# Kernel tuning notes

Measured on AMD Instinct MI355X. Metric: run time of the kernel, lower is better.

Reference implementation:

```python
import jax, jax.numpy as jnp
import numpy as np
from jax import lax

# Model dims (match init_kwargs / Mamba2 defaults)
B = 8; C_IN = 512; C_OUT = 512; H = 32; W = 32; L = H * W
D_STATE = 64; D_CONV = 4; EXPAND = 2; HEADDIM = 64
D_INNER = EXPAND * C_IN            # 1024
NHEADS = D_INNER // HEADDIM        # 16
D_XBC = D_INNER + 2 * D_STATE      # 1152 (ngroups=1)
D_IN_PROJ = 2 * D_INNER + 2 * D_STATE + NHEADS
EPS = 1e-5


def setup_inputs() -> dict:
    key = jax.random.key(0)
    ks = jax.random.split(key, 16)
    x = jax.random.normal(ks[0], (B, C_IN, H, W), jnp.float32)
    ln_w = jnp.ones((C_IN,), jnp.float32)
    ln_b = jnp.zeros((C_IN,), jnp.float32)
    in_proj_w = jax.random.normal(ks[1], (D_IN_PROJ, C_IN), jnp.float32) * 0.02
    conv1d_w = jax.random.normal(ks[2], (D_XBC, D_CONV), jnp.float32) * 0.2
    conv1d_b = jax.random.normal(ks[3], (D_XBC,), jnp.float32) * 0.02
    dt0 = jax.random.uniform(ks[4], (NHEADS,), jnp.float32, 1e-3, 0.1)
    dt_bias = jnp.log(jnp.expm1(dt0))  # inverse softplus init
    A_log = jnp.log(jax.random.uniform(ks[5], (NHEADS,), jnp.float32, 1.0, 16.0))
    D = jax.random.normal(ks[6], (NHEADS,), jnp.float32)
    rms_w = jnp.ones((D_INNER,), jnp.float32)
    out_proj_w = jax.random.normal(ks[7], (C_IN, D_INNER), jnp.float32) * 0.02
    conv2d_w = jax.random.normal(ks[8], (C_OUT, C_IN), jnp.float32) * 0.04
    conv2d_b = jnp.zeros((C_OUT,), jnp.float32)
    bn_g = jnp.ones((C_OUT,), jnp.float32)
    bn_b = jnp.zeros((C_OUT,), jnp.float32)
    bn_mean = jnp.zeros((C_OUT,), jnp.float32)
    bn_var = jnp.ones((C_OUT,), jnp.float32)
    return dict(x=x, ln_w=ln_w, ln_b=ln_b, in_proj_w=in_proj_w, conv1d_w=conv1d_w,
                conv1d_b=conv1d_b, dt_bias=dt_bias, A_log=A_log, D=D, rms_w=rms_w,
                out_proj_w=out_proj_w, conv2d_w=conv2d_w, conv2d_b=conv2d_b,
                bn_g=bn_g, bn_b=bn_b, bn_mean=bn_mean, bn_var=bn_var)


def reference(x, ln_w, ln_b, in_proj_w, conv1d_w, conv1d_b, dt_bias, A_log, D,
              rms_w, out_proj_w, conv2d_w, conv2d_b, bn_g, bn_b, bn_mean, bn_var):
    Bb, C, Hh, Ww = x.shape
    Ltok = Hh * Ww
    # tokens: (B, L, C)
    t = x.reshape(Bb, C, Ltok).transpose(0, 2, 1)
    # LayerNorm over channel dim
    mu = jnp.mean(t, -1, keepdims=True)
    var = jnp.mean(jnp.square(t - mu), -1, keepdims=True)
    xn = (t - mu) * lax.rsqrt(var + EPS) * ln_w + ln_b
    # Mamba2 in_proj -> [z, xBC, dt]
    zxbcdt = jnp.einsum('blc,dc->bld', xn, in_proj_w)
    z = zxbcdt[..., :D_INNER]
    xBC = zxbcdt[..., D_INNER:D_INNER + D_XBC]
    dt = zxbcdt[..., D_INNER + D_XBC:]                       # (B, L, nheads)
    # causal depthwise conv1d + silu
    conv = lax.conv_general_dilated(xBC.transpose(0, 2, 1), conv1d_w[:, None, :],
                                    window_strides=(1,), padding=[(D_CONV - 1, 0)],
                                    feature_group_count=D_XBC)
    xBC = jax.nn.silu(conv.transpose(0, 2, 1) + conv1d_b)
    xh = xBC[..., :D_INNER].reshape(Bb, Ltok, NHEADS, HEADDIM)
    Bm = xBC[..., D_INNER:D_INNER + D_STATE]                 # (B, L, d_state)
    Cm = xBC[..., D_INNER + D_STATE:]
    dt = jax.nn.softplus(dt + dt_bias)
    A = -jnp.exp(A_log)                                      # (nheads,)
    # selective scan (SSD recurrence), state h: (B, nheads, headdim, d_state)
    def step(h, inp):
        xt, dtt, Bt, Ct = inp
        dA = jnp.exp(dtt * A)                                # (B, nheads)
        h = h * dA[..., None, None] + jnp.einsum('bh,bhp,bs->bhps', dtt, xt, Bt)
        y = jnp.einsum('bhps,bs->bhp', h, Ct)
        return h, y
    h0 = jnp.zeros((Bb, NHEADS, HEADDIM, D_STATE), x.dtype)
    xs = (xh.transpose(1, 0, 2, 3), dt.transpose(1, 0, 2),
          Bm.transpose(1, 0, 2), Cm.transpose(1, 0, 2))
    _, ys = lax.scan(step, h0, xs)
    y = ys.transpose(1, 0, 2, 3) + D[None, None, :, None] * xh
    y = y.reshape(Bb, Ltok, D_INNER)
    # gated RMSNorm
    y = y * jax.nn.silu(z)
    y = y * lax.rsqrt(jnp.mean(y * y, -1, keepdims=True) + EPS) * rms_w
    out = jnp.einsum('bld,cd->blc', y, out_proj_w)
    img = out.transpose(0, 2, 1).reshape(Bb, C, Hh, Ww)
    # 1x1 conv + BN (inference) + ReLU
    c = jnp.einsum('bchw,oc->bohw', img, conv2d_w) + conv2d_b[None, :, None, None]
    c = (c - bn_mean[None, :, None, None]) * lax.rsqrt(bn_var + EPS)[None, :, None, None]
    c = c * bn_g[None, :, None, None] + bn_b[None, :, None, None]
    return jax.nn.relu(c)
```

## Files before the change

kernel.cpp:

```cpp
#include <hip/hip_runtime.h>
#include <hip/hip_bf16.h>

#define NB 8
#define LL 1024
#define CIN 512
#define DIN 1024
#define DXBC 1152
#define DPROJ 2192
#define NPADW 2304
#define NHH 16
#define HDD 64
#define DST 64
#define NCHUNK 16
#define QCH 64
#define XBCS 1024
#define CTT 8
#define DTB 16

typedef unsigned short u16;
typedef unsigned int u32;
typedef __bf16 bf16x8 __attribute__((ext_vector_type(8)));
typedef float f32x4 __attribute__((ext_vector_type(4)));
typedef u16 u16x8 __attribute__((ext_vector_type(8)));

__device__ __forceinline__ float bf2f(u16 u) {
    u32 x = ((u32)u) << 16; float f; __builtin_memcpy(&f, &x, 4); return f;
}
__device__ __forceinline__ u16 f2bf(float f) {
    u32 x; __builtin_memcpy(&x, &f, 4);
    u32 r = x + 0x7fff + ((x >> 16) & 1);
    return (u16)(r >> 16);
}

__device__ __forceinline__ void gload16(const u16* g, u16* l) {
    __builtin_amdgcn_global_load_lds((__attribute__((address_space(1))) void*)(g),
                                     (__attribute__((address_space(3))) void*)(l), 16, 0, 0);
}

__device__ __forceinline__ int swz(int row, int cb) {
    return row * 64 + ((cb ^ ((row & 7) << 4)) >> 1);
}

__global__ void f2bf_kernel(const float* __restrict__ s, u16* __restrict__ d, int n) {
    int i = blockIdx.x * 256 + threadIdx.x;
    if (i < n) d[i] = f2bf(s[i]);
}
__global__ void f2bf_pad(const float* __restrict__ s, u16* __restrict__ d, int nsrc, int ndst) {
    int i = blockIdx.x * 256 + threadIdx.x;
    if (i < ndst) d[i] = (i < nsrc) ? f2bf(s[i]) : (u16)0;
}
__global__ __launch_bounds__(256) void woutT_conv(const float* __restrict__ s,
                                                  const float* __restrict__ rw,
                                                  u16* __restrict__ dt) {
    __shared__ float tile[64][65];
    int bc = blockIdx.x & 7, bd = blockIdx.x >> 3;
    int c0 = bc * 64, d0 = bd * 64;
    int t = threadIdx.x;
    int r4 = t >> 6, cc = t & 63;
#pragma unroll
    for (int rr = 0; rr < 16; ++rr) {
        int row = r4 * 16 + rr;
        tile[row][cc] = s[(size_t)(c0 + row) * DIN + d0 + cc];
    }
    __syncthreads();
#pragma unroll
    for (int rr = 0; rr < 16; ++rr) {
        int row = r4 * 16 + rr;
        dt[(size_t)(d0 + row) * CIN + c0 + cc] = f2bf(tile[cc][row] * rw[d0 + row]);
    }
}
__global__ void bn_prep(const float* __restrict__ cb, const float* __restrict__ g,
                        const float* __restrict__ bb, const float* __restrict__ mean,
                        const float* __restrict__ var, float* __restrict__ scale,
                        float* __restrict__ shift) {
    int i = blockIdx.x * 256 + threadIdx.x;
    if (i < CIN) {
        float rs = rsqrtf(var[i] + 1e-5f);
        float sc = g[i] * rs;
        scale[i] = sc;
        shift[i] = (cb[i] - mean[i]) * sc + bb[i];
    }
}

__global__ __launch_bounds__(256) void ln_kernel(const float* __restrict__ x,
                                                 const float* __restrict__ lw,
                                                 const float* __restrict__ lb,
                                                 u16* __restrict__ xn) {
    __shared__ u16 tile[CIN * 33];
    __shared__ float psum[8][32], psq[8][32], muA[32], rsA[32];
    int bid = blockIdx.x;
    int b = bid >> 5, hw0 = (bid & 31) * 32;
    int t = threadIdx.x;
    int hw = t & 31, cg = t >> 5;
    const float* xb = x + (size_t)b * CIN * LL + hw0 + hw;
    float s = 0.f, sq = 0.f;
    for (int r = 0; r < CIN / 8; ++r) {
        int c = r * 8 + cg;
        float v = xb[(size_t)c * LL];
        s += v; sq += v * v;
        tile[c * 33 + hw] = f2bf(v);
    }
    psum[cg][hw] = s; psq[cg][hw] = sq;
    __syncthreads();
    if (t < 32) {
        float ss = 0.f, qq = 0.f;
        for (int g = 0; g < 8; ++g) { ss += psum[g][t]; qq += psq[g][t]; }
        float mu = ss * (1.f / CIN);
        float var = qq * (1.f / CIN) - mu * mu;
        muA[t] = mu; rsA[t] = rsqrtf(var + 1e-5f);
    }
    __syncthreads();
    for (int r = 0; r < 64; ++r) {
        int idx = r * 256 + t;
        int c = idx & (CIN - 1);
        int hh = idx >> 9;
        float v = (bf2f(tile[c * 33 + hh]) - muA[hh]) * rsA[hh] * lw[c] + lb[c];
        xn[((size_t)(b * LL + hw0 + hh)) * CIN + c] = f2bf(v);
    }
}

template <int EPI>
__global__ __launch_bounds__(256) void gemm_bt(const u16* __restrict__ A, const u16* __restrict__ Bw,
                                               void* __restrict__ Cout, int M, int N, int K, int ldc,
                                               int nx,
                                               const float* __restrict__ scale,
                                               const float* __restrict__ shift,
                                               const float* __restrict__ rsc) {
    __shared__ u16 As[2][128 * 64], Bs[2][64 * 64];
    int t = threadIdx.x;
    int lane = t & 63, wave = t >> 6;
    int nblk = gridDim.x;
    int qq = nblk >> 3, rm = nblk & 7;
    int xcd = blockIdx.x & 7, idx = blockIdx.x >> 3;
    int swzb = (xcd < rm ? xcd * (qq + 1) : rm * (qq + 1) + (xcd - rm) * qq) + idx;
    int m0 = (swzb / nx) * 128, n0 = (swzb % nx) * 64;
    int wr = wave >> 1, wc = wave & 1;
    f32x4 acc[4][2];
    for (int m = 0; m < 4; ++m)
        for (int n = 0; n < 2; ++n)
            for (int q = 0; q < 4; ++q) acc[m][n][q] = 0.f;

    const u16* Arow = A + (size_t)m0 * K;
    const u16* Brow = Bw + (size_t)n0 * K;
    int s4 = lane >> 4;
    int rr = lane & 15;

    auto STAGE = [&](int buf, int k0) {
#pragma unroll
        for (int j = 0; j < 4; ++j) {
            int e = j * 256 + t;
            int r = e >> 3, sr = e & 7;
            int src = (sr ^ (r & 7)) * 8;
            gload16(Arow + (size_t)r * K + k0 + src, &As[buf][e * 8]);
        }
#pragma unroll
        for (int j = 0; j < 2; ++j) {
            int e = j * 256 + t;
            int r = e >> 3, sr = e & 7;
            int src = (sr ^ (r & 7)) * 8;
            gload16(Brow + (size_t)r * K + k0 + src, &Bs[buf][e * 8]);
        }
    };

    STAGE(0, 0);
    int NK = K >> 6, cur = 0;
    for (int kt = 0; kt < NK; ++kt) {
        if (kt + 1 < NK) {
            STAGE(cur ^ 1, (kt + 1) << 6);
            asm volatile("s_waitcnt vmcnt(6)" ::: "memory");
        } else {
            asm volatile("s_waitcnt vmcnt(0)" ::: "memory");
        }
        __builtin_amdgcn_s_barrier();
        __builtin_amdgcn_sched_barrier(0);
#pragma unroll
        for (int kk = 0; kk < 2; ++kk) {
            bf16x8 af[4], bfr[2];
#pragma unroll
            for (int m = 0; m < 4; ++m) {
                int row = wr * 64 + m * 16 + rr;
                int ss = (kk * 4 + s4) ^ (row & 7);
                af[m] = *(const bf16x8*)&As[cur][row * 64 + ss * 8];
            }
#pragma unroll
            for (int n = 0; n < 2; ++n) {
                int row = wc * 32 + n * 16 + rr;
                int ss = (kk * 4 + s4) ^ (row & 7);
                bfr[n] = *(const bf16x8*)&Bs[cur][row * 64 + ss * 8];
            }
#pragma unroll
            for (int m = 0; m < 4; ++m)
#pragma unroll
                for (int n = 0; n < 2; ++n)
                    acc[m][n] = __builtin_amdgcn_mfma_f32_16x16x32_bf16(af[m], bfr[n], acc[m][n], 0, 0, 0);
        }
        __builtin_amdgcn_s_barrier();
        cur ^= 1;
    }
    int fq = lane >> 4, fr = lane & 15;
#pragma unroll
    for (int m = 0; m < 4; ++m) {
#pragma unroll
        for (int n = 0; n < 2; ++n) {
            int col = n0 + wc * 32 + n * 16 + fr;
#pragma unroll
            for (int q = 0; q < 4; ++q) {
                int row = m0 + wr * 64 + m * 16 + fq * 4 + q;
                float v = acc[m][n][q];
                if (EPI == 0) {
                    ((u16*)Cout)[(size_t)row * ldc + col] = f2bf(v);
                } else {
                    v = v * rsc[col];
                    v = v * scale[row] + shift[row];
                    v = v > 0.f ? v : 0.f;
                    ((float*)Cout)[((size_t)(col >> 10)) * (CIN * LL) + (size_t)row * LL + (col & 1023)] = v;
                }
            }
        }
    }
}

__global__ __launch_bounds__(288) void conv1d_fused(const u16* __restrict__ zx,
                                                    const float* __restrict__ w,
                                                    const float* __restrict__ bias,
                                                    u16* __restrict__ xbc,
                                                    u16* __restrict__ Bc, u16* __restrict__ Cc) {
    int bid = blockIdx.x;
    int b = bid >> 7;
    int l0 = (bid & 127) * CTT;
    int t = threadIdx.x;
    bool isX = t < 256;
    int ch = isX ? t * 4 : 1024 + (t - 256) * 4;

    float4 wv0 = *(const float4*)&w[(ch + 0) * 4];
    float4 wv1 = *(const float4*)&w[(ch + 1) * 4];
    float4 wv2 = *(const float4*)&w[(ch + 2) * 4];
    float4 wv3 = *(const float4*)&w[(ch + 3) * 4];
    float4 bv = *(const float4*)&bias[ch];

    ushort4 xin[CTT + 3];
    const u16* src = zx + (size_t)(b * LL + l0 - 3) * NPADW + DIN + ch;
#pragma unroll
    for (int i = 0; i < CTT + 3; ++i) {
        ushort4 v = {0, 0, 0, 0};
        if (l0 + i - 3 >= 0) v = *(const ushort4*)(src + (size_t)i * NPADW);
        xin[i] = v;
    }
#pragma unroll
    for (int i = 0; i < CTT; ++i) {
        int tok = b * LL + l0 + i;
        float a0 = bv.x + bf2f(xin[i].x) * wv0.x + bf2f(xin[i + 1].x) * wv0.y +
                   bf2f(xin[i + 2].x) * wv0.z + bf2f(xin[i + 3].x) * wv0.w;
        float a1 = bv.y + bf2f(xin[i].y) * wv1.x + bf2f(xin[i + 1].y) * wv1.y +
                   bf2f(xin[i + 2].y) * wv1.z + bf2f(xin[i + 3].y) * wv1.w;
        float a2 = bv.z + bf2f(xin[i].z) * wv2.x + bf2f(xin[i + 1].z) * wv2.y +
                   bf2f(xin[i + 2].z) * wv2.z + bf2f(xin[i + 3].z) * wv2.w;
        float a3 = bv.w + bf2f(xin[i].w) * wv3.x + bf2f(xin[i + 1].w) * wv3.y +
                   bf2f(xin[i + 2].w) * wv3.z + bf2f(xin[i + 3].w) * wv3.w;
        float s0 = a0 / (1.f + __expf(-a0));
        float s1 = a1 / (1.f + __expf(-a1));
        float s2 = a2 / (1.f + __expf(-a2));
        float s3 = a3 / (1.f + __expf(-a3));
        ushort4 o;
        o.x = f2bf(s0); o.y = f2bf(s1); o.z = f2bf(s2); o.w = f2bf(s3);
        if (isX) {
            *(ushort4*)&xbc[(size_t)tok * XBCS + ch] = o;
        } else {
            int s = ch - 1024;
            if (s < DST) *(ushort4*)&Bc[(size_t)tok * DST + s] = o;
            else         *(ushort4*)&Cc[(size_t)tok * DST + (s - DST)] = o;
        }
    }
}

__global__ __launch_bounds__(256) void dt_gemv(const u16* __restrict__ xn,
                                               const float* __restrict__ wproj,
                                               const float* __restrict__ dt_bias,
                                               const float* __restrict__ A_log,
                                               float2* __restrict__ dtda) {
    int t = threadIdx.x;
    int h = t >> 4, part = t & 15;
    int tok0 = blockIdx.x * DTB;
    const float* wr = wproj + (size_t)(DIN + DXBC + h) * CIN + part * 32;
    float4 w[8];
#pragma unroll
    for (int i = 0; i < 8; ++i) w[i] = *(const float4*)&wr[i * 4];
    const float* wf = (const float*)w;
    float dtb = dt_bias[h];
    float An = -__expf(A_log[h]);
#pragma unroll
    for (int tl = 0; tl < DTB; ++tl) {
        int tok = tok0 + tl;
        const u16* xr = xn + (size_t)tok * CIN + part * 32;
        u16x8 xv0 = *(const u16x8*)&xr[0];
        u16x8 xv1 = *(const u16x8*)&xr[8];
        u16x8 xv2 = *(const u16x8*)&xr[16];
        u16x8 xv3 = *(const u16x8*)&xr[24];
        float s = 0.f;
#pragma unroll
        for (int i = 0; i < 8; ++i) s += bf2f(xv0[i]) * wf[i];
#pragma unroll
        for (int i = 0; i < 8; ++i) s += bf2f(xv1[i]) * wf[8 + i];
#pragma unroll
        for (int i = 0; i < 8; ++i) s += bf2f(xv2[i]) * wf[16 + i];
#pragma unroll
        for (int i = 0; i < 8; ++i) s += bf2f(xv3[i]) * wf[24 + i];
        s += __shfl_xor(s, 1, 64);
        s += __shfl_xor(s, 2, 64);
        s += __shfl_xor(s, 4, 64);
        s += __shfl_xor(s, 8, 64);
        if (part == 0) {
            float si = s + dtb;
            float dtv = si > 15.f ? si : __logf(1.f + __expf(si));
            float2 dd; dd.x = dtv; dd.y = dtv * An;
            dtda[(size_t)tok * NHH + h] = dd;
        }
    }
}

__global__ __launch_bounds__(256) void ssd_chunk(const u16* __restrict__ Bcb,
                                                 const u16* __restrict__ Ccb,
                                                 const u16* __restrict__ xbc,
                                                 const float2* __restrict__ dtda,
                                                 u16* __restrict__ yi,
                                                 u16* __restrict__ DHb,
                                                 float* __restrict__ ESA,
                                                 float* __restrict__ DC) {
    __shared__ u16 Bt[4096], Ct[4096], XT[4096], BTt[4096], Gt[4096];
    __shared__ float Sar[64], dtvA[64], wA[64];
    int tau = blockIdx.x;
    int b = tau >> 8, h = (tau >> 4) & 15, c = tau & 15;
    int t0g = b * LL + c * QCH;
    int t = threadIdx.x, lane = t & 63, wave = t >> 6;
    int row = t >> 2, q = t & 3;

    {
        const u16* bp = Bcb + (size_t)(t0g + row) * DST + q * 16;
        const u16* cp = Ccb + (size_t)(t0g + row) * DST + q * 16;
        u16x8 b0v = *(const u16x8*)bp;
        u16x8 b1v = *(const u16x8*)(bp + 8);
        *(u16x8*)&Bt[swz(row, q * 32)] = b0v;
        *(u16x8*)&Bt[swz(row, q * 32 + 16)] = b1v;
        u16x8 c0v = *(const u16x8*)cp;
        u16x8 c1v = *(const u16x8*)(cp + 8);
        *(u16x8*)&Ct[swz(row, q * 32)] = c0v;
        *(u16x8*)&Ct[swz(row, q * 32 + 16)] = c1v;
        const u16* xp = xbc + (size_t)(t0g + row) * XBCS + h * HDD + q * 16;
        u16x8 x0 = *(const u16x8*)xp;
        u16x8 x1 = *(const u16x8*)(xp + 8);
#pragma unroll
        for (int e = 0; e < 8; ++e) XT[swz(q * 16 + e, row * 2)] = x0[e];
#pragma unroll
        for (int e = 0; e < 8; ++e) XT[swz(q * 16 + 8 + e, row * 2)] = x1[e];
    }
    if (t < 64) {
        float2 dd = dtda[(size_t)(t0g + t) * NHH + h];
        float s = dd.y;
#pragma unroll
        for (int off = 1; off < 64; off <<= 1) {
            float u = __shfl_up(s, off, 64);
            if (t >= off) s += u;
        }
        float SQ = __shfl(s, 63, 64);
        Sar[t] = s; dtvA[t] = dd.x;
        wA[t] = __expf(SQ - s) * dd.x;
        ESA[(size_t)tau * 64 + t] = __expf(s);
        if (t == 0) DC[tau] = __expf(SQ);
    }
    __syncthreads();

    int R = wave >> 1, Cq = wave & 1, rr = lane & 15, sg = lane >> 4;
    f32x4 g[2][2];
#pragma unroll
    for (int mi = 0; mi < 2; ++mi)
#pragma unroll
        for (int ni = 0; ni < 2; ++ni)
#pragma unroll
            for (int r = 0; r < 4; ++r) g[mi][ni][r] = 0.f;
#pragma unroll
    for (int kt = 0; kt < 2; ++kt) {
        int cb = kt * 64 + sg * 16;
        bf16x8 a0 = *(const bf16x8*)&Ct[swz(R * 32 + rr, cb)];
        bf16x8 a1 = *(const bf16x8*)&Ct[swz(R * 32 + 16 + rr, cb)];
        bf16x8 b0 = *(const bf16x8*)&Bt[swz(Cq * 32 + rr, cb)];
        bf16x8 b1 = *(const bf16x8*)&Bt[swz(Cq * 32 + 16 + rr, cb)];
        g[0][0] = __builtin_amdgcn_mfma_f32_16x16x32_bf16(a0, b0, g[0][0], 0, 0, 0);
        g[0][1] = __builtin_amdgcn_mfma_f32_16x16x32_bf16(a0, b1, g[0][1], 0, 0, 0);
        g[1][0] = __builtin_amdgcn_mfma_f32_16x16x32_bf16(a1, b0, g[1][0], 0, 0, 0);
        g[1][1] = __builtin_amdgcn_mfma_f32_16x16x32_bf16(a1, b1, g[1][1], 0, 0, 0);
    }
#pragma unroll
    for (int mi = 0; mi < 2; ++mi)
#pragma unroll
        for (int ni = 0; ni < 2; ++ni)
#pragma unroll
            for (int r = 0; r < 4; ++r) {
                int i = R * 32 + mi * 16 + sg * 4 + r;
                int j = Cq * 32 + ni * 16 + rr;
                float v = (i >= j) ? g[mi][ni][r] * __expf(Sar[i] - Sar[j]) * dtvA[j] : 0.f;
                Gt[swz(i, j * 2)] = f2bf(v);
            }
#pragma unroll
    for (int half = 0; half < 2; ++half) {
        u16x8 bv = *(const u16x8*)&Bt[swz(row, q * 32 + half * 16)];
#pragma unroll
        for (int e = 0; e < 8; ++e)
            BTt[swz(q * 16 + half * 8 + e, row * 2)] = f2bf(bf2f(bv[e]) * wA[row]);
    }
    __syncthreads();

    f32x4 y[2][2], dh[2][2];
#pragma unroll
    for (int mi = 0; mi < 2; ++mi)
#pragma unroll
        for (int ni = 0; ni < 2; ++ni)
#pragma unroll
            for (int r = 0; r < 4; ++r) { y[mi][ni][r] = 0.f; dh[mi][ni][r] = 0.f; }
#pragma unroll
    for (int kt = 0; kt < 2; ++kt) {
        int cb = kt * 64 + sg * 16;
        bf16x8 xb0 = *(const bf16x8*)&XT[swz(Cq * 32 + rr, cb)];
        bf16x8 xb1 = *(const bf16x8*)&XT[swz(Cq * 32 + 16 + rr, cb)];
        bf16x8 ga0 = *(const bf16x8*)&Gt[swz(R * 32 + rr, cb)];
        bf16x8 ga1 = *(const bf16x8*)&Gt[swz(R * 32 + 16 + rr, cb)];
        bf16x8 ba0 = *(const bf16x8*)&BTt[swz(R * 32 + rr, cb)];
        bf16x8 ba1 = *(const bf16x8*)&BTt[swz(R * 32 + 16 + rr, cb)];
        y[0][0] = __builtin_amdgcn_mfma_f32_16x16x32_bf16(ga0, xb0, y[0][0], 0, 0, 0);
        y[0][1] = __builtin_amdgcn_mfma_f32_16x16x32_bf16(ga0, xb1, y[0][1], 0, 0, 0);
        y[1][0] = __builtin_amdgcn_mfma_f32_16x16x32_bf16(ga1, xb0, y[1][0], 0, 0, 0);
        y[1][1] = __builtin_amdgcn_mfma_f32_16x16x32_bf16(ga1, xb1, y[1][1], 0, 0, 0);
        dh[0][0] = __builtin_amdgcn_mfma_f32_16x16x32_bf16(ba0, xb0, dh[0][0], 0, 0, 0);
        dh[0][1] = __builtin_amdgcn_mfma_f32_16x16x32_bf16(ba0, xb1, dh[0][1], 0, 0, 0);
        dh[1][0] = __builtin_amdgcn_mfma_f32_16x16x32_bf16(ba1, xb0, dh[1][0], 0, 0, 0);
        dh[1][1] = __builtin_amdgcn_mfma_f32_16x16x32_bf16(ba1, xb1, dh[1][1], 0, 0, 0);
    }
#pragma unroll
    for (int mi = 0; mi < 2; ++mi)
#pragma unroll
        for (int ni = 0; ni < 2; ++ni)
#pragma unroll
            for (int r = 0; r < 4; ++r) {
                int i = R * 32 + mi * 16 + sg * 4 + r;
                int p = Cq * 32 + ni * 16 + rr;
                yi[(size_t)(t0g + i) * DIN + h * HDD + p] = f2bf(y[mi][ni][r]);
                DHb[(size_t)tau * 4096 + i * 64 + p] = f2bf(dh[mi][ni][r]);
            }
}

__global__ __launch_bounds__(256) void ssd_carry(const u16* __restrict__ DHb,
                                                 const float* __restrict__ DC,
                                                 u16* __restrict__ HPREV) {
    int bid = blockIdx.x;
    int bh = bid >> 1, ph = bid & 1;
    int t = threadIdx.x;
    int s = t >> 2, p0 = ph * 32 + (t & 3) * 8;
    size_t base = (size_t)bh * NCHUNK * 4096 + s * 64 + p0;
    float Hv[8] = {0.f, 0.f, 0.f, 0.f, 0.f, 0.f, 0.f, 0.f};
    for (int c = 0; c < NCHUNK; ++c) {
        size_t off = base + (size_t)c * 4096;
        u16x8 hp;
#pragma unroll
        for (int e = 0; e < 8; ++e) hp[e] = f2bf(Hv[e]);
        *(u16x8*)&HPREV[off] = hp;
        float d = DC[bh * NCHUNK + c];
        u16x8 dv = *(const u16x8*)&DHb[off];
#pragma unroll
        for (int e = 0; e < 8; ++e) Hv[e] = d * Hv[e] + bf2f(dv[e]);
    }
}

__global__ __launch_bounds__(256) void ssd_final(const u16* __restrict__ Ccb,
                                                 const float* __restrict__ ESA,
                                                 const u16* __restrict__ HPREV,
                                                 const u16* __restrict__ xbc,
                                                 const u16* __restrict__ zx,
                                                 const float* __restrict__ Dp,
                                                 u16* __restrict__ yi,
                                                 float* __restrict__ PS) {
    __shared__ u16 C2t[4096], HT[4096];
    __shared__ float smem_ps[2][64];
    int tau = blockIdx.x;
    int b = tau >> 8, h = (tau >> 4) & 15, c = tau & 15;
    int t0g = b * LL + c * QCH;
    int t = threadIdx.x, lane = t & 63, wave = t >> 6;
    int row = t >> 2, q = t & 3;
    {
        float esa = ESA[(size_t)tau * 64 + row];
        const u16* cp = Ccb + (size_t)(t0g + row) * DST + q * 16;
#pragma unroll
        for (int half = 0; half < 2; ++half) {
            u16x8 cv = *(const u16x8*)(cp + half * 8);
            u16x8 oc;
#pragma unroll
            for (int e = 0; e < 8; ++e) oc[e] = f2bf(bf2f(cv[e]) * esa);
            *(u16x8*)&C2t[swz(row, q * 32 + half * 16)] = oc;
            u16x8 hv = *(const u16x8*)&HPREV[(size_t)tau * 4096 + row * 64 + q * 16 + half * 8];
#pragma unroll
            for (int e = 0; e < 8; ++e) HT[swz(q * 16 + half * 8 + e, row * 2)] = hv[e];
        }
    }
    __syncthreads();
    int R = wave >> 1, Cq = wave & 1, rr = lane & 15, sg = lane >> 4;
    float Dh = Dp[h];
    f32x4 acc[2][2];
#pragma unroll
    for (int mi = 0; mi < 2; ++mi)
#pragma unroll
        for (int ni = 0; ni < 2; ++ni)
#pragma unroll
            for (int r = 0; r < 4; ++r) {
                int i = R * 32 + mi * 16 + sg * 4 + r;
                int p = Cq * 32 + ni * 16 + rr;
                acc[mi][ni][r] = bf2f(yi[(size_t)(t0g + i) * DIN + h * HDD + p]);
            }
#pragma unroll
    for (int kt = 0; kt < 2; ++kt) {
        int cb = kt * 64 + sg * 16;
        bf16x8 a0 = *(const bf16x8*)&C2t[swz(R * 32 + rr, cb)];
        bf16x8 a1 = *(const bf16x8*)&C2t[swz(R * 32 + 16 + rr, cb)];
        bf16x8 b0 = *(const bf16x8*)&HT[swz(Cq * 32 + rr, cb)];
        bf16x8 b1 = *(const bf16x8*)&HT[swz(Cq * 32 + 16 + rr, cb)];
        acc[0][0] = __builtin_amdgcn_mfma_f32_16x16x32_bf16(a0, b0, acc[0][0], 0, 0, 0);
        acc[0][1] = __builtin_amdgcn_mfma_f32_16x16x32_bf16(a0, b1, acc[0][1], 0, 0, 0);
        acc[1][0] = __builtin_amdgcn_mfma_f32_16x16x32_bf16(a1, b0, acc[1][0], 0, 0, 0);
        acc[1][1] = __builtin_amdgcn_mfma_f32_16x16x32_bf16(a1, b1, acc[1][1], 0, 0, 0);
    }
    float ps[2][4];
#pragma unroll
    for (int mi = 0; mi < 2; ++mi)
#pragma unroll
        for (int r = 0; r < 4; ++r) ps[mi][r] = 0.f;
#pragma unroll
    for (int mi = 0; mi < 2; ++mi)
#pragma unroll
        for (int ni = 0; ni < 2; ++ni)
#pragma unroll
            for (int r = 0; r < 4; ++r) {
                int i = R * 32 + mi * 16 + sg * 4 + r;
                int p = Cq * 32 + ni * 16 + rr;
                size_t tok = t0g + i;
                int col = h * HDD + p;
                float xf = bf2f(xbc[tok * XBCS + col]);
                float zf = bf2f(zx[tok * NPADW + col]);
                float yo = (acc[mi][ni][r] + Dh * xf) * (zf / (1.f + __expf(-zf)));
                yi[tok * DIN + col] = f2bf(yo);
                ps[mi][r] += yo * yo;
            }
#pragma unroll
    for (int mi = 0; mi < 2; ++mi)
#pragma unroll
        for (int r = 0; r < 4; ++r) {
            float s2 = ps[mi][r];
            s2 += __shfl_xor(s2, 1, 64);
            s2 += __shfl_xor(s2, 2, 64);
            s2 += __shfl_xor(s2, 4, 64);
            s2 += __shfl_xor(s2, 8, 64);
            if (rr == 0) smem_ps[Cq][R * 32 + mi * 16 + sg * 4 + r] = s2;
        }
    __syncthreads();
    if (t < 64) PS[(size_t)tau * 64 + t] = smem_ps[0][t] + smem_ps[1][t];
}

__global__ __launch_bounds__(256) void rs_from_ps(const float* __restrict__ PS,
                                                  float* __restrict__ RS) {
    int tok = blockIdx.x * 256 + threadIdx.x;
    int b = tok >> 10, rem = tok & 1023;
    int c = rem >> 6, i = rem & 63;
    float s = 0.f;
#pragma unroll
    for (int h = 0; h < NHH; ++h)
        s += PS[(size_t)(((b << 4) + h) * 16 + c) * 64 + i];
    RS[tok] = rsqrtf(s * (1.f / DIN) + 1e-5f);
}

extern "C" void kernel_launch(void* const* d_in, const int* in_sizes, int n_in,
                              void* d_out, int out_size, void* d_ws, size_t ws_size,
                              hipStream_t stream) {
    const float* x         = (const float*)d_in[0];
    const float* ln_w      = (const float*)d_in[1];
    const float* ln_b      = (const float*)d_in[2];
    const float* in_proj_w = (const float*)d_in[3];
    const float* conv1d_w  = (const float*)d_in[4];
    const float* conv1d_b  = (const float*)d_in[5];
    const float* dt_bias   = (const float*)d_in[6];
    const float* A_log     = (const float*)d_in[7];
    const float* Dp        = (const float*)d_in[8];
    const float* rms_w     = (const float*)d_in[9];
    const float* out_proj_w= (const float*)d_in[10];
    const float* conv2d_w  = (const float*)d_in[11];
    const float* conv2d_b  = (const float*)d_in[12];
    const float* bn_g      = (const float*)d_in[13];
    const float* bn_b      = (const float*)d_in[14];
    const float* bn_mean   = (const float*)d_in[15];
    const float* bn_var    = (const float*)d_in[16];

    const int TOK = NB * LL;
    const int NTAU = NB * NHH * NCHUNK;
    char* ws = (char*)d_ws;
    size_t off = 0;
    auto alloc = [&](size_t bytes) {
        void* p = ws + off;
        off += (bytes + 255) & ~(size_t)255;
        return p;
    };
    u16*   Win   = (u16*)alloc((size_t)NPADW * CIN * 2);
    u16*   WoutT = (u16*)alloc((size_t)DIN * CIN * 2);
    u16*   Wc2   = (u16*)alloc((size_t)CIN * CIN * 2);
    u16*   WCMB  = (u16*)alloc((size_t)CIN * DIN * 2);
    u16*   XN    = (u16*)alloc((size_t)TOK * CIN * 2);
    u16*   ZX    = (u16*)alloc((size_t)TOK * NPADW * 2);
    u16*   XBC   = (u16*)alloc((size_t)TOK * XBCS * 2);
    u16*   Bcb   = (u16*)alloc((size_t)TOK * DST * 2);
    u16*   Ccb   = (u16*)alloc((size_t)TOK * DST * 2);
    float2* DTDA = (float2*)alloc((size_t)TOK * NHH * 8);
    u16*   YI    = (u16*)alloc((size_t)TOK * DIN * 2);
    u16*   DHb   = (u16*)alloc((size_t)NTAU * 4096 * 2);
    u16*   HPREV = (u16*)alloc((size_t)NTAU * 4096 * 2);
    float* ESA   = (float*)alloc((size_t)NTAU * 64 * 4);
    float* PS    = (float*)alloc((size_t)NTAU * 64 * 4);
    float* DC    = (float*)alloc((size_t)NTAU * 4);
    float* RS    = (float*)alloc((size_t)TOK * 4);
    float* BNSC  = (float*)alloc(CIN * 4);
    float* BNSH  = (float*)alloc(CIN * 4);

    f2bf_pad<<<(NPADW * CIN + 255) / 256, 256, 0, stream>>>(in_proj_w, Win, DPROJ * CIN, NPADW * CIN);
    woutT_conv<<<128, 256, 0, stream>>>(out_proj_w, rms_w, WoutT);
    f2bf_kernel<<<(CIN * CIN + 255) / 256, 256, 0, stream>>>(conv2d_w, Wc2, CIN * CIN);
    bn_prep<<<2, 256, 0, stream>>>(conv2d_b, bn_g, bn_b, bn_mean, bn_var, BNSC, BNSH);
    gemm_bt<0><<<(CIN / 128) * (DIN / 64), 256, 0, stream>>>(Wc2, WoutT, WCMB, CIN, DIN, CIN, DIN,
                                                             DIN / 64, nullptr, nullptr, nullptr);

    ln_kernel<<<256, 256, 0, stream>>>(x, ln_w, ln_b, XN);

    gemm_bt<0><<<(TOK / 128) * (NPADW / 64), 256, 0, stream>>>(XN, Win, ZX, TOK, NPADW, CIN, NPADW,
                                                               NPADW / 64, nullptr, nullptr, nullptr);

    conv1d_fused<<<NB * (LL / CTT), 288, 0, stream>>>(ZX, conv1d_w, conv1d_b, XBC, Bcb, Ccb);
    dt_gemv<<<TOK / DTB, 256, 0, stream>>>(XN, in_proj_w, dt_bias, A_log, DTDA);

    ssd_chunk<<<NTAU, 256, 0, stream>>>(Bcb, Ccb, XBC, DTDA, YI, DHb, ESA, DC);
    ssd_carry<<<256, 256, 0, stream>>>(DHb, DC, HPREV);
    ssd_final<<<NTAU, 256, 0, stream>>>(Ccb, ESA, HPREV, XBC, ZX, Dp, YI, PS);

    rs_from_ps<<<TOK / 256, 256, 0, stream>>>(PS, RS);

    gemm_bt<1><<<(CIN / 128) * (TOK / 64), 256, 0, stream>>>(WCMB, YI, d_out, CIN, TOK, DIN, 0,
                                                             TOK / 64, BNSC, BNSH, RS);
}
```

Before: 152.4 us.

## Use 128x128 GEMM tiles with BK=32 and repacked swizzled LDS layout

```diff
diff --git a/kernel.cpp b/kernel.cpp
--- a/kernel.cpp
+++ b/kernel.cpp
@@ -126,18 +126,18 @@
                                                const float* __restrict__ scale,
                                                const float* __restrict__ shift,
                                                const float* __restrict__ rsc) {
-    __shared__ u16 As[2][128 * 64], Bs[2][64 * 64];
+    __shared__ u16 As[2][64 * 64], Bs[2][64 * 64];
     int t = threadIdx.x;
     int lane = t & 63, wave = t >> 6;
     int nblk = gridDim.x;
     int qq = nblk >> 3, rm = nblk & 7;
     int xcd = blockIdx.x & 7, idx = blockIdx.x >> 3;
     int swzb = (xcd < rm ? xcd * (qq + 1) : rm * (qq + 1) + (xcd - rm) * qq) + idx;
-    int m0 = (swzb / nx) * 128, n0 = (swzb % nx) * 64;
+    int m0 = (swzb / nx) * 128, n0 = (swzb % nx) * 128;
     int wr = wave >> 1, wc = wave & 1;
-    f32x4 acc[4][2];
+    f32x4 acc[4][4];
     for (int m = 0; m < 4; ++m)
-        for (int n = 0; n < 2; ++n)
+        for (int n = 0; n < 4; ++n)
             for (int q = 0; q < 4; ++q) acc[m][n][q] = 0.f;
 
     const u16* Arow = A + (size_t)m0 * K;
@@ -147,53 +147,58 @@
 
     auto STAGE = [&](int buf, int k0) {
 #pragma unroll
-        for (int j = 0; j < 4; ++j) {
-            int e = j * 256 + t;
-            int r = e >> 3, sr = e & 7;
-            int src = (sr ^ (r & 7)) * 8;
-            gload16(Arow + (size_t)r * K + k0 + src, &As[buf][e * 8]);
-        }
-#pragma unroll
         for (int j = 0; j < 2; ++j) {
             int e = j * 256 + t;
-            int r = e >> 3, sr = e & 7;
-            int src = (sr ^ (r & 7)) * 8;
-            gload16(Brow + (size_t)r * K + k0 + src, &Bs[buf][e * 8]);
+            int R = e >> 3, Sp = e & 7;
+            int S = Sp ^ (R & 7);
+            int row = R * 2 + (S >> 2);
+            int kc = S & 3;
+            gload16(Arow + (size_t)row * K + k0 + kc * 8, &As[buf][e * 8]);
+        }
+#pragma unroll
+        for (int j = 0; j < 2; ++j) {
+            int e = j * 256 + t;
+            int R = e >> 3, Sp = e & 7;
+            int S = Sp ^ (R & 7);
+            int row = R * 2 + (S >> 2);
+            int kc = S & 3;
+            gload16(Brow + (size_t)row * K + k0 + kc * 8, &Bs[buf][e * 8]);
         }
     };
 
     STAGE(0, 0);
-    int NK = K >> 6, cur = 0;
+    int NK = K >> 5, cur = 0;
     for (int kt = 0; kt < NK; ++kt) {
         if (kt + 1 < NK) {
-            STAGE(cur ^ 1, (kt + 1) << 6);
-            asm volatile("s_waitcnt vmcnt(6)" ::: "memory");
+            STAGE(cur ^ 1, (kt + 1) << 5);
+            asm volatile("s_waitcnt vmcnt(4)" ::: "memory");
         } else {
             asm volatile("s_waitcnt vmcnt(0)" ::: "memory");
         }
         __builtin_amdgcn_s_barrier();
         __builtin_amdgcn_sched_barrier(0);
-#pragma unroll
-        for (int kk = 0; kk < 2; ++kk) {
-            bf16x8 af[4], bfr[2];
-#pragma unroll
-            for (int m = 0; m < 4; ++m) {
-                int row = wr * 64 + m * 16 + rr;
-                int ss = (kk * 4 + s4) ^ (row & 7);
-                af[m] = *(const bf16x8*)&As[cur][row * 64 + ss * 8];
-            }
-#pragma unroll
-            for (int n = 0; n < 2; ++n) {
-                int row = wc * 32 + n * 16 + rr;
-                int ss = (kk * 4 + s4) ^ (row & 7);
-                bfr[n] = *(const bf16x8*)&Bs[cur][row * 64 + ss * 8];
-            }
-#pragma unroll
-            for (int m = 0; m < 4; ++m)
-#pragma unroll
-                for (int n = 0; n < 2; ++n)
-                    acc[m][n] = __builtin_amdgcn_mfma_f32_16x16x32_bf16(af[m], bfr[n], acc[m][n], 0, 0, 0);
-        }
+        bf16x8 af[4], bfr[4];
+#pragma unroll
+        for (int m = 0; m < 4; ++m) {
+            int row = wr * 64 + m * 16 + rr;
+            int R = row >> 1;
+            int S = ((row & 1) << 2) | s4;
+            int Sp = S ^ (R & 7);
+            af[m] = *(const bf16x8*)&As[cur][R * 64 + Sp * 8];
+        }
+#pragma unroll
+        for (int n = 0; n < 4; ++n) {
+            int row = wc * 64 + n * 16 + rr;
+            int R = row >> 1;
+            int S = ((row & 1) << 2) | s4;
+            int Sp = S ^ (R & 7);
+            bfr[n] = *(const bf16x8*)&Bs[cur][R * 64 + Sp * 8];
+        }
+#pragma unroll
+        for (int m = 0; m < 4; ++m)
+#pragma unroll
+            for (int n = 0; n < 4; ++n)
+                acc[m][n] = __builtin_amdgcn_mfma_f32_16x16x32_bf16(af[m], bfr[n], acc[m][n], 0, 0, 0);
         __builtin_amdgcn_s_barrier();
         cur ^= 1;
     }
@@ -201,8 +206,8 @@
 #pragma unroll
     for (int m = 0; m < 4; ++m) {
 #pragma unroll
-        for (int n = 0; n < 2; ++n) {
-            int col = n0 + wc * 32 + n * 16 + fr;
+        for (int n = 0; n < 4; ++n) {
+            int col = n0 + wc * 64 + n * 16 + fr;
 #pragma unroll
             for (int q = 0; q < 4; ++q) {
                 int row = m0 + wr * 64 + m * 16 + fq * 4 + q;
@@ -627,13 +632,13 @@
     woutT_conv<<<128, 256, 0, stream>>>(out_proj_w, rms_w, WoutT);
     f2bf_kernel<<<(CIN * CIN + 255) / 256, 256, 0, stream>>>(conv2d_w, Wc2, CIN * CIN);
     bn_prep<<<2, 256, 0, stream>>>(conv2d_b, bn_g, bn_b, bn_mean, bn_var, BNSC, BNSH);
-    gemm_bt<0><<<(CIN / 128) * (DIN / 64), 256, 0, stream>>>(Wc2, WoutT, WCMB, CIN, DIN, CIN, DIN,
-                                                             DIN / 64, nullptr, nullptr, nullptr);
+    gemm_bt<0><<<(CIN / 128) * (DIN / 128), 256, 0, stream>>>(Wc2, WoutT, WCMB, CIN, DIN, CIN, DIN,
+                                                              DIN / 128, nullptr, nullptr, nullptr);
 
     ln_kernel<<<256, 256, 0, stream>>>(x, ln_w, ln_b, XN);
 
-    gemm_bt<0><<<(TOK / 128) * (NPADW / 64), 256, 0, stream>>>(XN, Win, ZX, TOK, NPADW, CIN, NPADW,
-                                                               NPADW / 64, nullptr, nullptr, nullptr);
+    gemm_bt<0><<<(TOK / 128) * (NPADW / 128), 256, 0, stream>>>(XN, Win, ZX, TOK, NPADW, CIN, NPADW,
+                                                                NPADW / 128, nullptr, nullptr, nullptr);
 
     conv1d_fused<<<NB * (LL / CTT), 288, 0, stream>>>(ZX, conv1d_w, conv1d_b, XBC, Bcb, Ccb);
     dt_gemv<<<TOK / DTB, 256, 0, stream>>>(XN, in_proj_w, dt_bias, A_log, DTDA);
@@ -644,6 +649,6 @@
 
     rs_from_ps<<<TOK / 256, 256, 0, stream>>>(PS, RS);
 
-    gemm_bt<1><<<(CIN / 128) * (TOK / 64), 256, 0, stream>>>(WCMB, YI, d_out, CIN, TOK, DIN, 0,
-                                                             TOK / 64, BNSC, BNSH, RS);
-}
+    gemm_bt<1><<<(CIN / 128) * (TOK / 128), 256, 0, stream>>>(WCMB, YI, d_out, CIN, TOK, DIN, 0,
+                                                              TOK / 128, BNSC, BNSH, RS);
+}
```

Result: slower. 162.0 us (+6.3%).

## Merge prep, conv/dt and RMS kernels into fewer launches; trim in-proj GEMM columns

Applied to the files above, without the earlier changes.

```diff
diff --git a/kernel.cpp b/kernel.cpp
--- a/kernel.cpp
+++ b/kernel.cpp
@@ -8,6 +8,7 @@
 #define DXBC 1152
 #define DPROJ 2192
 #define NPADW 2304
+#define NUSE 2176
 #define NHH 16
 #define HDD 64
 #define DST 64
@@ -41,14 +42,32 @@
     return row * 64 + ((cb ^ ((row & 7) << 4)) >> 1);
 }
 
-__global__ void f2bf_kernel(const float* __restrict__ s, u16* __restrict__ d, int n) {
-    int i = blockIdx.x * 256 + threadIdx.x;
-    if (i < n) d[i] = f2bf(s[i]);
-}
-__global__ void f2bf_pad(const float* __restrict__ s, u16* __restrict__ d, int nsrc, int ndst) {
-    int i = blockIdx.x * 256 + threadIdx.x;
-    if (i < ndst) d[i] = (i < nsrc) ? f2bf(s[i]) : (u16)0;
-}
+#define PREP_WIN_BLKS 4608
+#define PREP_WC2_BLKS 1024
+__global__ __launch_bounds__(256) void prep_all(const float* __restrict__ ipw, u16* __restrict__ Win,
+                                                const float* __restrict__ c2w, u16* __restrict__ Wc2,
+                                                const float* __restrict__ cb, const float* __restrict__ g,
+                                                const float* __restrict__ bb, const float* __restrict__ mean,
+                                                const float* __restrict__ var,
+                                                float* __restrict__ scale, float* __restrict__ shift) {
+    int bid = blockIdx.x;
+    if (bid < PREP_WIN_BLKS) {
+        int i = bid * 256 + threadIdx.x;
+        Win[i] = (i < DPROJ * CIN) ? f2bf(ipw[i]) : (u16)0;
+    } else if (bid < PREP_WIN_BLKS + PREP_WC2_BLKS) {
+        int i = (bid - PREP_WIN_BLKS) * 256 + threadIdx.x;
+        Wc2[i] = f2bf(c2w[i]);
+    } else {
+        int i = (bid - PREP_WIN_BLKS - PREP_WC2_BLKS) * 256 + threadIdx.x;
+        if (i < CIN) {
+            float rs = rsqrtf(var[i] + 1e-5f);
+            float sc = g[i] * rs;
+            scale[i] = sc;
+            shift[i] = (cb[i] - mean[i]) * sc + bb[i];
+        }
+    }
+}
+
 __global__ __launch_bounds__(256) void woutT_conv(const float* __restrict__ s,
                                                   const float* __restrict__ rw,
                                                   u16* __restrict__ dt) {
@@ -67,18 +86,6 @@
     for (int rr = 0; rr < 16; ++rr) {
         int row = r4 * 16 + rr;
         dt[(size_t)(d0 + row) * CIN + c0 + cc] = f2bf(tile[cc][row] * rw[d0 + row]);
-    }
-}
-__global__ void bn_prep(const float* __restrict__ cb, const float* __restrict__ g,
-                        const float* __restrict__ bb, const float* __restrict__ mean,
-                        const float* __restrict__ var, float* __restrict__ scale,
-                        float* __restrict__ shift) {
-    int i = blockIdx.x * 256 + threadIdx.x;
-    if (i < CIN) {
-        float rs = rsqrtf(var[i] + 1e-5f);
-        float sc = g[i] * rs;
-        scale[i] = sc;
-        shift[i] = (cb[i] - mean[i]) * sc + bb[i];
     }
 }
 
@@ -125,8 +132,9 @@
                                                int nx,
                                                const float* __restrict__ scale,
                                                const float* __restrict__ shift,
-                                               const float* __restrict__ rsc) {
+                                               const float* __restrict__ PS) {
     __shared__ u16 As[2][128 * 64], Bs[2][64 * 64];
+    __shared__ float rsl[64];
     int t = threadIdx.x;
     int lane = t & 63, wave = t >> 6;
     int nblk = gridDim.x;
@@ -140,6 +148,20 @@
         for (int n = 0; n < 2; ++n)
             for (int q = 0; q < 4; ++q) acc[m][n][q] = 0.f;
 
+    if (EPI == 1) {
+        if (t < 64) {
+            int tok = n0 + t;
+            int b = tok >> 10, rem = tok & 1023;
+            int c = rem >> 6, ii = rem & 63;
+            float s = 0.f;
+#pragma unroll
+            for (int h = 0; h < NHH; ++h)
+                s += PS[(size_t)(((b << 4) + h) * 16 + c) * 64 + ii];
+            rsl[t] = rsqrtf(s * (1.f / DIN) + 1e-5f);
+        }
+        __syncthreads();
+    }
+
     const u16* Arow = A + (size_t)m0 * K;
     const u16* Brow = Bw + (size_t)n0 * K;
     int s4 = lane >> 4;
@@ -210,7 +232,7 @@
                 if (EPI == 0) {
                     ((u16*)Cout)[(size_t)row * ldc + col] = f2bf(v);
                 } else {
-                    v = v * rsc[col];
+                    v = v * rsl[col - n0];
                     v = v * scale[row] + shift[row];
                     v = v > 0.f ? v : 0.f;
                     ((float*)Cout)[((size_t)(col >> 10)) * (CIN * LL) + (size_t)row * LL + (col & 1023)] = v;
@@ -220,100 +242,101 @@
     }
 }
 
-__global__ __launch_bounds__(288) void conv1d_fused(const u16* __restrict__ zx,
-                                                    const float* __restrict__ w,
-                                                    const float* __restrict__ bias,
-                                                    u16* __restrict__ xbc,
-                                                    u16* __restrict__ Bc, u16* __restrict__ Cc) {
+__global__ __launch_bounds__(288) void convdt(const u16* __restrict__ zx,
+                                              const float* __restrict__ w,
+                                              const float* __restrict__ bias,
+                                              u16* __restrict__ xbc,
+                                              u16* __restrict__ Bc, u16* __restrict__ Cc,
+                                              const u16* __restrict__ xn,
+                                              const float* __restrict__ wproj,
+                                              const float* __restrict__ dt_bias,
+                                              const float* __restrict__ A_log,
+                                              float2* __restrict__ dtda) {
     int bid = blockIdx.x;
-    int b = bid >> 7;
-    int l0 = (bid & 127) * CTT;
     int t = threadIdx.x;
-    bool isX = t < 256;
-    int ch = isX ? t * 4 : 1024 + (t - 256) * 4;
-
-    float4 wv0 = *(const float4*)&w[(ch + 0) * 4];
-    float4 wv1 = *(const float4*)&w[(ch + 1) * 4];
-    float4 wv2 = *(const float4*)&w[(ch + 2) * 4];
-    float4 wv3 = *(const float4*)&w[(ch + 3) * 4];
-    float4 bv = *(const float4*)&bias[ch];
-
-    ushort4 xin[CTT + 3];
-    const u16* src = zx + (size_t)(b * LL + l0 - 3) * NPADW + DIN + ch;
-#pragma unroll
-    for (int i = 0; i < CTT + 3; ++i) {
-        ushort4 v = {0, 0, 0, 0};
-        if (l0 + i - 3 >= 0) v = *(const ushort4*)(src + (size_t)i * NPADW);
-        xin[i] = v;
-    }
-#pragma unroll
-    for (int i = 0; i < CTT; ++i) {
-        int tok = b * LL + l0 + i;
-        float a0 = bv.x + bf2f(xin[i].x) * wv0.x + bf2f(xin[i + 1].x) * wv0.y +
-                   bf2f(xin[i + 2].x) * wv0.z + bf2f(xin[i + 3].x) * wv0.w;
-        float a1 = bv.y + bf2f(xin[i].y) * wv1.x + bf2f(xin[i + 1].y) * wv1.y +
-                   bf2f(xin[i + 2].y) * wv1.z + bf2f(xin[i + 3].y) * wv1.w;
-        float a2 = bv.z + bf2f(xin[i].z) * wv2.x + bf2f(xin[i + 1].z) * wv2.y +
-                   bf2f(xin[i + 2].z) * wv2.z + bf2f(xin[i + 3].z) * wv2.w;
-        float a3 = bv.w + bf2f(xin[i].w) * wv3.x + bf2f(xin[i + 1].w) * wv3.y +
-                   bf2f(xin[i + 2].w) * wv3.z + bf2f(xin[i + 3].w) * wv3.w;
-        float s0 = a0 / (1.f + __expf(-a0));
-        float s1 = a1 / (1.f + __expf(-a1));
-        float s2 = a2 / (1.f + __expf(-a2));
-        float s3 = a3 / (1.f + __expf(-a3));
-        ushort4 o;
-        o.x = f2bf(s0); o.y = f2bf(s1); o.z = f2bf(s2); o.w = f2bf(s3);
-        if (isX) {
-            *(ushort4*)&xbc[(size_t)tok * XBCS + ch] = o;
-        } else {
-            int s = ch - 1024;
-            if (s < DST) *(ushort4*)&Bc[(size_t)tok * DST + s] = o;
-            else         *(ushort4*)&Cc[(size_t)tok * DST + (s - DST)] = o;
-        }
-    }
-}
-
-__global__ __launch_bounds__(256) void dt_gemv(const u16* __restrict__ xn,
-                                               const float* __restrict__ wproj,
-                                               const float* __restrict__ dt_bias,
-                                               const float* __restrict__ A_log,
-                                               float2* __restrict__ dtda) {
-    int t = threadIdx.x;
-    int h = t >> 4, part = t & 15;
-    int tok0 = blockIdx.x * DTB;
-    const float* wr = wproj + (size_t)(DIN + DXBC + h) * CIN + part * 32;
-    float4 w[8];
-#pragma unroll
-    for (int i = 0; i < 8; ++i) w[i] = *(const float4*)&wr[i * 4];
-    const float* wf = (const float*)w;
-    float dtb = dt_bias[h];
-    float An = -__expf(A_log[h]);
-#pragma unroll
-    for (int tl = 0; tl < DTB; ++tl) {
-        int tok = tok0 + tl;
-        const u16* xr = xn + (size_t)tok * CIN + part * 32;
-        u16x8 xv0 = *(const u16x8*)&xr[0];
-        u16x8 xv1 = *(const u16x8*)&xr[8];
-        u16x8 xv2 = *(const u16x8*)&xr[16];
-        u16x8 xv3 = *(const u16x8*)&xr[24];
-        float s = 0.f;
-#pragma unroll
-        for (int i = 0; i < 8; ++i) s += bf2f(xv0[i]) * wf[i];
-#pragma unroll
-        for (int i = 0; i < 8; ++i) s += bf2f(xv1[i]) * wf[8 + i];
-#pragma unroll
-        for (int i = 0; i < 8; ++i) s += bf2f(xv2[i]) * wf[16 + i];
-#pragma unroll
-        for (int i = 0; i < 8; ++i) s += bf2f(xv3[i]) * wf[24 + i];
-        s += __shfl_xor(s, 1, 64);
-        s += __shfl_xor(s, 2, 64);
-        s += __shfl_xor(s, 4, 64);
-        s += __shfl_xor(s, 8, 64);
-        if (part == 0) {
-            float si = s + dtb;
-            float dtv = si > 15.f ? si : __logf(1.f + __expf(si));
-            float2 dd; dd.x = dtv; dd.y = dtv * An;
-            dtda[(size_t)tok * NHH + h] = dd;
+    if (bid < NB * (LL / CTT)) {
+        int b = bid >> 7;
+        int l0 = (bid & 127) * CTT;
+        bool isX = t < 256;
+        int ch = isX ? t * 4 : 1024 + (t - 256) * 4;
+
+        float4 wv0 = *(const float4*)&w[(ch + 0) * 4];
+        float4 wv1 = *(const float4*)&w[(ch + 1) * 4];
+        float4 wv2 = *(const float4*)&w[(ch + 2) * 4];
+        float4 wv3 = *(const float4*)&w[(ch + 3) * 4];
+        float4 bv = *(const float4*)&bias[ch];
+
+        ushort4 xin[CTT + 3];
+        const u16* src = zx + (size_t)(b * LL + l0 - 3) * NPADW + DIN + ch;
+#pragma unroll
+        for (int i = 0; i < CTT + 3; ++i) {
+            ushort4 v = {0, 0, 0, 0};
+            if (l0 + i - 3 >= 0) v = *(const ushort4*)(src + (size_t)i * NPADW);
+            xin[i] = v;
+        }
+#pragma unroll
+        for (int i = 0; i < CTT; ++i) {
+            int tok = b * LL + l0 + i;
+            float a0 = bv.x + bf2f(xin[i].x) * wv0.x + bf2f(xin[i + 1].x) * wv0.y +
+                       bf2f(xin[i + 2].x) * wv0.z + bf2f(xin[i + 3].x) * wv0.w;
+            float a1 = bv.y + bf2f(xin[i].y) * wv1.x + bf2f(xin[i + 1].y) * wv1.y +
+                       bf2f(xin[i + 2].y) * wv1.z + bf2f(xin[i + 3].y) * wv1.w;
+            float a2 = bv.z + bf2f(xin[i].z) * wv2.x + bf2f(xin[i + 1].z) * wv2.y +
+                       bf2f(xin[i + 2].z) * wv2.z + bf2f(xin[i + 3].z) * wv2.w;
+            float a3 = bv.w + bf2f(xin[i].w) * wv3.x + bf2f(xin[i + 1].w) * wv3.y +
+                       bf2f(xin[i + 2].w) * wv3.z + bf2f(xin[i + 3].w) * wv3.w;
+            float s0 = a0 / (1.f + __expf(-a0));
+            float s1 = a1 / (1.f + __expf(-a1));
+            float s2 = a2 / (1.f + __expf(-a2));
+            float s3 = a3 / (1.f + __expf(-a3));
+            ushort4 o;
+            o.x = f2bf(s0); o.y = f2bf(s1); o.z = f2bf(s2); o.w = f2bf(s3);
+            if (isX) {
+                *(ushort4*)&xbc[(size_t)tok * XBCS + ch] = o;
+            } else {
+                int s = ch - 1024;
+                if (s < DST) *(ushort4*)&Bc[(size_t)tok * DST + s] = o;
+                else         *(ushort4*)&Cc[(size_t)tok * DST + (s - DST)] = o;
+            }
+        }
+    } else {
+        if (t >= 256) return;
+        int h = t >> 4, part = t & 15;
+        int tok0 = (bid - NB * (LL / CTT)) * DTB;
+        const float* wr = wproj + (size_t)(DIN + DXBC + h) * CIN + part * 32;
+        float4 wv[8];
+#pragma unroll
+        for (int i = 0; i < 8; ++i) wv[i] = *(const float4*)&wr[i * 4];
+        const float* wf = (const float*)wv;
+        float dtb = dt_bias[h];
+        float An = -__expf(A_log[h]);
+#pragma unroll
+        for (int tl = 0; tl < DTB; ++tl) {
+            int tok = tok0 + tl;
+            const u16* xr = xn + (size_t)tok * CIN + part * 32;
+            u16x8 xv0 = *(const u16x8*)&xr[0];
+            u16x8 xv1 = *(const u16x8*)&xr[8];
+            u16x8 xv2 = *(const u16x8*)&xr[16];
+            u16x8 xv3 = *(const u16x8*)&xr[24];
+            float s = 0.f;
+#pragma unroll
+            for (int i = 0; i < 8; ++i) s += bf2f(xv0[i]) * wf[i];
+#pragma unroll
+            for (int i = 0; i < 8; ++i) s += bf2f(xv1[i]) * wf[8 + i];
+#pragma unroll
+            for (int i = 0; i < 8; ++i) s += bf2f(xv2[i]) * wf[16 + i];
+#pragma unroll
+            for (int i = 0; i < 8; ++i) s += bf2f(xv3[i]) * wf[24 + i];
+            s += __shfl_xor(s, 1, 64);
+            s += __shfl_xor(s, 2, 64);
+            s += __shfl_xor(s, 4, 64);
+            s += __shfl_xor(s, 8, 64);
+            if (part == 0) {
+                float si = s + dtb;
+                float dtv = si > 15.f ? si : __logf(1.f + __expf(si));
+                float2 dd; dd.x = dtv; dd.y = dtv * An;
+                dtda[(size_t)tok * NHH + h] = dd;
+            }
         }
     }
 }
@@ -559,18 +582,6 @@
         }
     __syncthreads();
     if (t < 64) PS[(size_t)tau * 64 + t] = smem_ps[0][t] + smem_ps[1][t];
-}
-
-__global__ __launch_bounds__(256) void rs_from_ps(const float* __restrict__ PS,
-                                                  float* __restrict__ RS) {
-    int tok = blockIdx.x * 256 + threadIdx.x;
-    int b = tok >> 10, rem = tok & 1023;
-    int c = rem >> 6, i = rem & 63;
-    float s = 0.f;
-#pragma unroll
-    for (int h = 0; h < NHH; ++h)
-        s += PS[(size_t)(((b << 4) + h) * 16 + c) * 64 + i];
-    RS[tok] = rsqrtf(s * (1.f / DIN) + 1e-5f);
 }
 
 extern "C" void kernel_launch(void* const* d_in, const int* in_sizes, int n_in,
@@ -619,31 +630,27 @@
     float* ESA   = (float*)alloc((size_t)NTAU * 64 * 4);
     float* PS    = (float*)alloc((size_t)NTAU * 64 * 4);
     float* DC    = (float*)alloc((size_t)NTAU * 4);
-    float* RS    = (float*)alloc((size_t)TOK * 4);
     float* BNSC  = (float*)alloc(CIN * 4);
     float* BNSH  = (float*)alloc(CIN * 4);
 
-    f2bf_pad<<<(NPADW * CIN + 255) / 256, 256, 0, stream>>>(in_proj_w, Win, DPROJ * CIN, NPADW * CIN);
+    prep_all<<<PREP_WIN_BLKS + PREP_WC2_BLKS + 2, 256, 0, stream>>>(
+        in_proj_w, Win, conv2d_w, Wc2, conv2d_b, bn_g, bn_b, bn_mean, bn_var, BNSC, BNSH);
     woutT_conv<<<128, 256, 0, stream>>>(out_proj_w, rms_w, WoutT);
-    f2bf_kernel<<<(CIN * CIN + 255) / 256, 256, 0, stream>>>(conv2d_w, Wc2, CIN * CIN);
-    bn_prep<<<2, 256, 0, stream>>>(conv2d_b, bn_g, bn_b, bn_mean, bn_var, BNSC, BNSH);
     gemm_bt<0><<<(CIN / 128) * (DIN / 64), 256, 0, stream>>>(Wc2, WoutT, WCMB, CIN, DIN, CIN, DIN,
                                                              DIN / 64, nullptr, nullptr, nullptr);
 
     ln_kernel<<<256, 256, 0, stream>>>(x, ln_w, ln_b, XN);
 
-    gemm_bt<0><<<(TOK / 128) * (NPADW / 64), 256, 0, stream>>>(XN, Win, ZX, TOK, NPADW, CIN, NPADW,
-                                                               NPADW / 64, nullptr, nullptr, nullptr);
-
-    conv1d_fused<<<NB * (LL / CTT), 288, 0, stream>>>(ZX, conv1d_w, conv1d_b, XBC, Bcb, Ccb);
-    dt_gemv<<<TOK / DTB, 256, 0, stream>>>(XN, in_proj_w, dt_bias, A_log, DTDA);
+    gemm_bt<0><<<(TOK / 128) * (NUSE / 64), 256, 0, stream>>>(XN, Win, ZX, TOK, NUSE, CIN, NPADW,
+                                                              NUSE / 64, nullptr, nullptr, nullptr);
+
+    convdt<<<NB * (LL / CTT) + TOK / DTB, 288, 0, stream>>>(ZX, conv1d_w, conv1d_b, XBC, Bcb, Ccb,
+                                                            XN, in_proj_w, dt_bias, A_log, DTDA);
 
     ssd_chunk<<<NTAU, 256, 0, stream>>>(Bcb, Ccb, XBC, DTDA, YI, DHb, ESA, DC);
     ssd_carry<<<256, 256, 0, stream>>>(DHb, DC, HPREV);
     ssd_final<<<NTAU, 256, 0, stream>>>(Ccb, ESA, HPREV, XBC, ZX, Dp, YI, PS);
 
-    rs_from_ps<<<TOK / 256, 256, 0, stream>>>(PS, RS);
-
     gemm_bt<1><<<(CIN / 128) * (TOK / 64), 256, 0, stream>>>(WCMB, YI, d_out, CIN, TOK, DIN, 0,
-                                                             TOK / 64, BNSC, BNSH, RS);
-}
+                                                             TOK / 64, BNSC, BNSH, PS);
+}
```

Result: faster. 143.5 us (median of 2 runs) (-5.9%).
